# Kernel tuning notes

Measured on AMD Instinct MI355X. Metric: run time of the kernel, lower is better.

## Reference

```python
import jax, jax.numpy as jnp
import numpy as np

EPS = 1e-5  # torch InstanceNorm2d default eps

def conv1x1(x, w, b):
    # x: [B,C,H,W], w: [O,C], b: [O]
    return jnp.einsum('bchw,oc->bohw', x, w) + b[None, :, None, None]

def instance_norm(x):
    # InstanceNorm2d(affine=False): normalize per-sample, per-channel over H,W
    mean = jnp.mean(x, axis=(2, 3), keepdims=True)
    var = jnp.var(x, axis=(2, 3), keepdims=True)
    return (x - mean) * jax.lax.rsqrt(var + EPS)

def proj(x, w, b):
    return jax.nn.relu(instance_norm(conv1x1(x, w, b)))

def setup_inputs() -> dict:
    key = jax.random.key(0)
    ks = jax.random.split(key, 9)
    B, C, Ci, H, W = 16, 256, 128, 64, 64
    s_in = 1.0 / np.sqrt(C)
    s_mid = 1.0 / np.sqrt(Ci)
    return {
        'x': jax.random.normal(ks[0], (B, C, H, W), jnp.float32),
        'g_w': jax.random.normal(ks[1], (Ci, C), jnp.float32) * s_in,
        'g_b': jax.random.normal(ks[2], (Ci,), jnp.float32) * s_in,
        'theta_w': jax.random.normal(ks[3], (Ci, C), jnp.float32) * s_in,
        'theta_b': jax.random.normal(ks[4], (Ci,), jnp.float32) * s_in,
        'phi_w': jax.random.normal(ks[5], (Ci, C), jnp.float32) * s_in,
        'phi_b': jax.random.normal(ks[6], (Ci,), jnp.float32) * s_in,
        'W_w': jax.random.normal(ks[7], (C, Ci), jnp.float32) * s_mid,
        'W_b': jax.random.normal(ks[8], (C,), jnp.float32) * s_mid,
    }

def reference(x, g_w, g_b, theta_w, theta_b, phi_w, phi_b, W_w, W_b):
    B, C, H, W = x.shape
    Ci = g_w.shape[0]
    N = H * W
    g_x = proj(x, g_w, g_b).reshape(B, Ci, N)        # [B,Ci,N]
    theta_x = proj(x, theta_w, theta_b).reshape(B, Ci, N)
    phi_x = proj(x, phi_w, phi_b).reshape(B, Ci, N)
    # channel-attention Gram matrix [B,Ci,Ci], softmax over last dim
    f = jnp.einsum('bin,bjn->bij', theta_x, phi_x)
    attn = jax.nn.softmax(f, axis=2)
    y = jnp.einsum('bij,bjn->bin', attn, g_x)        # [B,Ci,N]
    # replicate torch permute(0,2,1).contiguous().view(B,Ci,H,W)
    y = jnp.transpose(y, (0, 2, 1)).reshape(B, Ci, H, W)
    y = instance_norm(conv1x1(y, W_w, W_b))
    return y + x
```

## Files before the change

kernel.cpp:

```cpp
#include <hip/hip_runtime.h>

#define DEVINL __device__ __forceinline__

typedef __attribute__((ext_vector_type(8))) short bf8v;
typedef __attribute__((ext_vector_type(4))) float f32x4;
typedef __attribute__((ext_vector_type(8))) unsigned short us8;
typedef __attribute__((ext_vector_type(4))) unsigned short us4;

DEVINL unsigned short f2bf(float f) {
  unsigned int u = __builtin_bit_cast(unsigned int, f);
  u += 0x7fffu + ((u >> 16) & 1u);
  return (unsigned short)(u >> 16);
}
DEVINL unsigned short f2bf_trunc(float f) {
  return (unsigned short)(__builtin_bit_cast(unsigned int, f) >> 16);
}
DEVINL float bf2f(unsigned short h) {
  unsigned int u = ((unsigned int)h) << 16;
  return __builtin_bit_cast(float, u);
}

__global__ __launch_bounds__(512, 2)
void proj_gemm(const unsigned short* __restrict__ wall_hi,
               const unsigned short* __restrict__ wall_lo,
               const float* __restrict__ x, float* __restrict__ z)
{
  __shared__ __align__(16) unsigned short As_hi[384 * 72];
  __shared__ __align__(16) unsigned short As_lo[256 * 72];
  __shared__ __align__(16) unsigned short Bs_hi[128 * 72];
  __shared__ __align__(16) unsigned short Bs_lo[128 * 72];

  const int t = threadIdx.x;
  const int lane = t & 63;
  const int wave = t >> 6;
  const int wm = wave >> 1, wn = wave & 1;
  const int lr = lane & 15, lk = lane >> 4;
  const int b = blockIdx.z;
  const int nbase = blockIdx.x * 128;
  const float* xs = x + (long)b * 256 * 4096;

  f32x4 acc[6][4];
#pragma unroll
  for (int i = 0; i < 6; ++i)
#pragma unroll
    for (int j = 0; j < 4; ++j) acc[i][j] = (f32x4)0.0f;

  for (int kt = 0; kt < 4; ++kt) {
    const int k0 = kt * 64;
#pragma unroll
    for (int i = 0; i < 6; ++i) {
      const int q = i * 512 + t;
      const int row = q >> 3, c = q & 7;
      *(us8*)&As_hi[row * 72 + c * 8] = *(const us8*)&wall_hi[(long)row * 256 + k0 + c * 8];
    }
#pragma unroll
    for (int i = 0; i < 4; ++i) {
      const int q = i * 512 + t;
      const int row = q >> 3, c = q & 7;
      *(us8*)&As_lo[row * 72 + c * 8] = *(const us8*)&wall_lo[(long)row * 256 + k0 + c * 8];
    }
    const int nl = t & 127, cg = t >> 7;
    float xv[16];
#pragma unroll
    for (int i = 0; i < 16; ++i)
      xv[i] = xs[(long)(k0 + cg * 16 + i) * 4096 + nbase + nl];
#pragma unroll
    for (int ch = 0; ch < 2; ++ch) {
      us8 h8, l8;
#pragma unroll
      for (int e = 0; e < 8; ++e) {
        const float v = xv[ch * 8 + e];
        const unsigned short hb = f2bf(v);
        h8[e] = hb;
        l8[e] = f2bf_trunc(v - bf2f(hb));
      }
      *(us8*)&Bs_hi[nl * 72 + cg * 16 + ch * 8] = h8;
      *(us8*)&Bs_lo[nl * 72 + cg * 16 + ch * 8] = l8;
    }
    __syncthreads();
#pragma unroll
    for (int ks = 0; ks < 2; ++ks) {
      const int ko = ks * 32 + lk * 8;
      bf8v bh[4], bl[4];
#pragma unroll
      for (int ni = 0; ni < 4; ++ni) {
        const int r = (wn * 64 + ni * 16 + lr) * 72 + ko;
        bh[ni] = *(const bf8v*)&Bs_hi[r];
        bl[ni] = *(const bf8v*)&Bs_lo[r];
      }
#pragma unroll
      for (int mi = 0; mi < 6; ++mi) {
        const int fr = mi * 4 + wm;
        const int r = (fr * 16 + lr) * 72 + ko;
        const bf8v ah = *(const bf8v*)&As_hi[r];
        if (fr < 16) {
          const bf8v al = *(const bf8v*)&As_lo[r];
#pragma unroll
          for (int ni = 0; ni < 4; ++ni) {
            acc[mi][ni] = __builtin_amdgcn_mfma_f32_16x16x32_bf16(bh[ni], ah, acc[mi][ni], 0, 0, 0);
            acc[mi][ni] = __builtin_amdgcn_mfma_f32_16x16x32_bf16(bl[ni], ah, acc[mi][ni], 0, 0, 0);
            acc[mi][ni] = __builtin_amdgcn_mfma_f32_16x16x32_bf16(bh[ni], al, acc[mi][ni], 0, 0, 0);
          }
        } else {
#pragma unroll
          for (int ni = 0; ni < 4; ++ni)
            acc[mi][ni] = __builtin_amdgcn_mfma_f32_16x16x32_bf16(bh[ni], ah, acc[mi][ni], 0, 0, 0);
        }
      }
    }
    __syncthreads();
  }
#pragma unroll
  for (int mi = 0; mi < 6; ++mi)
#pragma unroll
    for (int ni = 0; ni < 4; ++ni) {
      const int gm = (mi * 4 + wm) * 16 + lr;
      const int gn = nbase + wn * 64 + ni * 16 + lk * 4;
      *(f32x4*)&z[((long)b * 384 + gm) * 4096 + gn] = acc[mi][ni];
    }
}

template<int PASSES, bool OUT_BF16>
__global__ __launch_bounds__(256, 2)
void gemm_tn(const unsigned short* __restrict__ Ahi, const unsigned short* __restrict__ Alo,
             const unsigned short* __restrict__ Bhi, const unsigned short* __restrict__ Blo,
             void* __restrict__ Cout,
             int lda, int ldb, int ldc, int ksteps, int z1count,
             long aS1, long aS2, long bS1, long bS2, long cS1, long cS2)
{
  __shared__ __align__(16) unsigned short smem[(PASSES == 3 ? 4 : 2) * 128 * 72];
  unsigned short* As_hi = smem;
  unsigned short* Bs_hi = smem + 128 * 72;
  unsigned short* As_lo = smem + 2 * 128 * 72;
  unsigned short* Bs_lo = smem + 3 * 128 * 72;

  const int t = threadIdx.x;
  const int lane = t & 63;
  const int wave = t >> 6;
  const int wm = wave >> 1, wn = wave & 1;
  const int lr = lane & 15, lk = lane >> 4;

  const int z = blockIdx.z;
  const int zb = z / z1count, z1 = z - zb * z1count;
  const unsigned short* Ah = Ahi + zb * aS2 + z1 * aS1;
  const unsigned short* Bh = Bhi + zb * bS2 + z1 * bS1;
  const unsigned short* Al = (PASSES == 3) ? (Alo + zb * aS2 + z1 * aS1) : nullptr;
  const unsigned short* Bl = (PASSES == 3) ? (Blo + zb * bS2 + z1 * bS1) : nullptr;
  const long cOff = zb * cS2 + z1 * cS1;

  const int mbase = blockIdx.y * 128;
  const int nbase = blockIdx.x * 128;

  f32x4 acc[4][4];
#pragma unroll
  for (int i = 0; i < 4; ++i)
#pragma unroll
    for (int j = 0; j < 4; ++j) acc[i][j] = (f32x4)0.0f;

  for (int kt = 0; kt < ksteps; ++kt) {
    const int k0 = kt * 64;
#pragma unroll
    for (int i = 0; i < 4; ++i) {
      const int q = i * 256 + t;
      const int row = q >> 3, c = q & 7;
      const int lo = row * 72 + c * 8;
      *(us8*)&As_hi[lo] = *(const us8*)&Ah[(long)(mbase + row) * lda + k0 + c * 8];
      *(us8*)&Bs_hi[lo] = *(const us8*)&Bh[(long)(nbase + row) * ldb + k0 + c * 8];
      if (PASSES == 3) {
        *(us8*)&As_lo[lo] = *(const us8*)&Al[(long)(mbase + row) * lda + k0 + c * 8];
        *(us8*)&Bs_lo[lo] = *(const us8*)&Bl[(long)(nbase + row) * ldb + k0 + c * 8];
      }
    }
    __syncthreads();
#pragma unroll
    for (int ks = 0; ks < 2; ++ks) {
      const int ko = ks * 32 + lk * 8;
      bf8v ah[4], bh[4], al[4], bl[4];
#pragma unroll
      for (int mi = 0; mi < 4; ++mi) {
        const int r = (wm * 64 + mi * 16 + lr) * 72 + ko;
        ah[mi] = *(const bf8v*)&As_hi[r];
        if (PASSES == 3) al[mi] = *(const bf8v*)&As_lo[r];
      }
#pragma unroll
      for (int ni = 0; ni < 4; ++ni) {
        const int r = (wn * 64 + ni * 16 + lr) * 72 + ko;
        bh[ni] = *(const bf8v*)&Bs_hi[r];
        if (PASSES == 3) bl[ni] = *(const bf8v*)&Bs_lo[r];
      }
#pragma unroll
      for (int mi = 0; mi < 4; ++mi)
#pragma unroll
        for (int ni = 0; ni < 4; ++ni) {
          acc[mi][ni] = __builtin_amdgcn_mfma_f32_16x16x32_bf16(bh[ni], ah[mi], acc[mi][ni], 0, 0, 0);
          if (PASSES == 3) {
            acc[mi][ni] = __builtin_amdgcn_mfma_f32_16x16x32_bf16(bl[ni], ah[mi], acc[mi][ni], 0, 0, 0);
            acc[mi][ni] = __builtin_amdgcn_mfma_f32_16x16x32_bf16(bh[ni], al[mi], acc[mi][ni], 0, 0, 0);
          }
        }
    }
    __syncthreads();
  }

#pragma unroll
  for (int mi = 0; mi < 4; ++mi)
#pragma unroll
    for (int ni = 0; ni < 4; ++ni) {
      const int gm = mbase + wm * 64 + mi * 16 + lr;
      const int gn = nbase + wn * 64 + ni * 16 + lk * 4;
      const f32x4 v = acc[mi][ni];
      if (OUT_BF16) {
        us4 o;
#pragma unroll
        for (int r = 0; r < 4; ++r) o[r] = f2bf(v[r]);
        *(us4*)&((unsigned short*)Cout)[cOff + (long)gm * ldc + gn] = o;
      } else {
        *(f32x4*)&((float*)Cout)[cOff + (long)gm * ldc + gn] = v;
      }
    }
}

__global__ __launch_bounds__(256)
void prep_weights(const float* __restrict__ g_w, const float* __restrict__ th_w,
                  const float* __restrict__ ph_w, const float* __restrict__ W_w,
                  unsigned short* __restrict__ wall_hi, unsigned short* __restrict__ wall_lo,
                  unsigned short* __restrict__ w2h)
{
  const int i = blockIdx.x * 256 + threadIdx.x;
  float v;
  if (i < 32768) v = th_w[i];
  else if (i < 65536) v = ph_w[i - 32768];
  else v = g_w[i - 65536];
  const unsigned short h = f2bf(v);
  wall_hi[i] = h;
  if (i < 65536) wall_lo[i] = f2bf_trunc(v - bf2f(h));
  if (i < 32768) w2h[i] = f2bf(W_w[i]);
}

__global__ __launch_bounds__(256)
void norm_split(const float* __restrict__ z,
                unsigned short* __restrict__ nhi, unsigned short* __restrict__ nlo)
{
  const int row = blockIdx.x;
  const int b = row >> 8, m = row & 255;
  const float* src = z + ((long)b * 384 + m) * 4096;
  const int t = threadIdx.x;
  f32x4 v[4];
  float s = 0.f, ss = 0.f;
#pragma unroll
  for (int i = 0; i < 4; ++i) {
    v[i] = *(const f32x4*)&src[i * 1024 + t * 4];
#pragma unroll
    for (int e = 0; e < 4; ++e) { s += v[i][e]; ss += v[i][e] * v[i][e]; }
  }
  __shared__ float r0[256], r1[256];
  r0[t] = s; r1[t] = ss;
  __syncthreads();
  for (int o = 128; o > 0; o >>= 1) {
    if (t < o) { r0[t] += r0[t + o]; r1[t] += r1[t + o]; }
    __syncthreads();
  }
  const float mean = r0[0] * (1.f / 4096.f);
  const float var = r1[0] * (1.f / 4096.f) - mean * mean;
  const float rs = rsqrtf(fmaxf(var, 0.f) + 1e-5f);
  const long obase = (long)row * 4096;
#pragma unroll
  for (int i = 0; i < 4; ++i) {
    us4 hi, lo;
#pragma unroll
    for (int e = 0; e < 4; ++e) {
      const float nv = fmaxf((v[i][e] - mean) * rs, 0.f);
      const unsigned short h = f2bf(nv);
      hi[e] = h;
      lo[e] = f2bf_trunc(nv - bf2f(h));
    }
    *(us4*)&nhi[obase + i * 1024 + t * 4] = hi;
    *(us4*)&nlo[obase + i * 1024 + t * 4] = lo;
  }
}

__global__ __launch_bounds__(256)
void stats_g(const float* __restrict__ z, float* __restrict__ statsg)
{
  const int row = blockIdx.x;
  const int b = row >> 7, j = row & 127;
  const float* src = z + ((long)b * 384 + 256 + j) * 4096;
  const int t = threadIdx.x;
  float s = 0.f, ss = 0.f;
#pragma unroll
  for (int i = 0; i < 4; ++i) {
    f32x4 v = *(const f32x4*)&src[i * 1024 + t * 4];
#pragma unroll
    for (int e = 0; e < 4; ++e) { s += v[e]; ss += v[e] * v[e]; }
  }
  __shared__ float r0[256], r1[256];
  r0[t] = s; r1[t] = ss;
  __syncthreads();
  for (int o = 128; o > 0; o >>= 1) {
    if (t < o) { r0[t] += r0[t + o]; r1[t] += r1[t + o]; }
    __syncthreads();
  }
  if (t == 0) {
    const float mean = r0[0] * (1.f / 4096.f);
    const float var = r1[0] * (1.f / 4096.f) - mean * mean;
    statsg[row * 2] = mean;
    statsg[row * 2 + 1] = rsqrtf(fmaxf(var, 0.f) + 1e-5f);
  }
}

__global__ __launch_bounds__(256)
void norm_transpose_g(const float* __restrict__ z, const float* __restrict__ statsg,
                      unsigned short* __restrict__ gT)
{
  __shared__ unsigned short T[64 * 136];
  const int b = blockIdx.y, n0 = blockIdx.x * 64;
  const int t = threadIdx.x;
  const int c = t >> 1, part = t & 1;
  const float mu = statsg[(b * 128 + c) * 2];
  const float rs = statsg[(b * 128 + c) * 2 + 1];
  const float* src = z + ((long)b * 384 + 256 + c) * 4096 + n0 + part * 32;
#pragma unroll
  for (int j = 0; j < 8; ++j) {
    f32x4 v = *(const f32x4*)&src[j * 4];
#pragma unroll
    for (int e = 0; e < 4; ++e) {
      const float nv = fmaxf((v[e] - mu) * rs, 0.f);
      T[(part * 32 + j * 4 + e) * 136 + c] = f2bf(nv);
    }
  }
  __syncthreads();
  const int nl = t >> 2, q = t & 3;
  const long obase = ((long)b * 4096 + n0 + nl) * 128 + q * 32;
#pragma unroll
  for (int k = 0; k < 4; ++k) {
    us8 o;
#pragma unroll
    for (int e = 0; e < 8; ++e) o[e] = T[nl * 136 + q * 32 + k * 8 + e];
    *(us8*)&gT[obase + k * 8] = o;
  }
}

__global__ __launch_bounds__(64)
void softmax_attn(const float* __restrict__ fpart, unsigned short* __restrict__ attn)
{
  const int row = blockIdx.x;
  const int b = row >> 7, i = row & 127;
  const int t = threadIdx.x;
  float v0 = 0.f, v1 = 0.f;
#pragma unroll
  for (int kc = 0; kc < 32; ++kc) {
    const float* p = fpart + ((long)(b * 32 + kc)) * 16384 + i * 128;
    v0 += p[t];
    v1 += p[t + 64];
  }
  float mx = fmaxf(v0, v1);
  for (int o = 32; o > 0; o >>= 1) mx = fmaxf(mx, __shfl_xor(mx, o));
  const float e0 = __expf(v0 - mx), e1 = __expf(v1 - mx);
  float s = e0 + e1;
  for (int o = 32; o > 0; o >>= 1) s += __shfl_xor(s, o);
  const float inv = 1.f / s;
  attn[(long)row * 128 + t] = f2bf(e0 * inv);
  attn[(long)row * 128 + t + 64] = f2bf(e1 * inv);
}

__global__ __launch_bounds__(256)
void finalize(const unsigned short* __restrict__ z2b, const float* __restrict__ x,
              float* __restrict__ out)
{
  const int row = blockIdx.x;
  const long base = (long)row * 4096;
  const int t = threadIdx.x;
  float v[16];
  float s = 0.f, ss = 0.f;
#pragma unroll
  for (int h = 0; h < 2; ++h) {
    us8 u = *(const us8*)&z2b[base + t * 16 + h * 8];
#pragma unroll
    for (int e = 0; e < 8; ++e) {
      const float f = bf2f(u[e]);
      v[h * 8 + e] = f;
      s += f; ss += f * f;
    }
  }
  __shared__ float r0[256], r1[256];
  r0[t] = s; r1[t] = ss;
  __syncthreads();
  for (int o = 128; o > 0; o >>= 1) {
    if (t < o) { r0[t] += r0[t + o]; r1[t] += r1[t + o]; }
    __syncthreads();
  }
  const float mean = r0[0] * (1.f / 4096.f);
  const float var = r1[0] * (1.f / 4096.f) - mean * mean;
  const float rs = rsqrtf(fmaxf(var, 0.f) + 1e-5f);
#pragma unroll
  for (int i = 0; i < 4; ++i) {
    f32x4 xr = *(const f32x4*)&x[base + t * 16 + i * 4];
    f32x4 o;
#pragma unroll
    for (int e = 0; e < 4; ++e) o[e] = (v[i * 4 + e] - mean) * rs + xr[e];
    *(f32x4*)&out[base + t * 16 + i * 4] = o;
  }
}

extern "C" void kernel_launch(void* const* d_in, const int* in_sizes, int n_in,
                              void* d_out, int out_size, void* d_ws, size_t ws_size,
                              hipStream_t stream)
{
  const float* x    = (const float*)d_in[0];
  const float* g_w  = (const float*)d_in[1];
  const float* th_w = (const float*)d_in[3];
  const float* ph_w = (const float*)d_in[5];
  const float* W_w  = (const float*)d_in[7];

  char* ws = (char*)d_ws;
  const size_t MB = 1024ull * 1024ull;
  if (ws_size < 186 * MB) return;

  unsigned short* znorm_hi = (unsigned short*)(ws);
  unsigned short* znorm_lo = (unsigned short*)(ws + 32 * MB);
  float*          z_all    = (float*)(ws + 64 * MB);
  float*          fpart    = (float*)(ws + 64 * MB);
  unsigned short* attn     = (unsigned short*)(ws + 96 * MB);
  unsigned short* y4T      = (unsigned short*)(ws + 98 * MB);
  unsigned short* z2b      = (unsigned short*)(ws + 114 * MB);
  unsigned short* gT       = (unsigned short*)(ws + 160 * MB);
  unsigned short* wall_hi  = (unsigned short*)(ws + 176 * MB);
  unsigned short* wall_lo  = (unsigned short*)(ws + 176 * MB + 256 * 1024);
  unsigned short* w2h      = (unsigned short*)(ws + 176 * MB + 512 * 1024);
  float*          statsg   = (float*)(ws + 176 * MB + 640 * 1024);

  prep_weights<<<dim3(384), 256, 0, stream>>>(g_w, th_w, ph_w, W_w, wall_hi, wall_lo, w2h);

  proj_gemm<<<dim3(32, 1, 16), 512, 0, stream>>>(wall_hi, wall_lo, x, z_all);

  norm_split<<<dim3(4096), 256, 0, stream>>>(z_all, znorm_hi, znorm_lo);

  stats_g<<<dim3(2048), 256, 0, stream>>>(z_all, statsg);
  norm_transpose_g<<<dim3(64, 16), 256, 0, stream>>>(z_all, statsg, gT);

  gemm_tn<3, false><<<dim3(1, 1, 512), 256, 0, stream>>>(
      znorm_hi, znorm_lo, znorm_hi + (long)128 * 4096, znorm_lo + (long)128 * 4096, fpart,
      4096, 4096, 128, 2, 32,
      128, (long)256 * 4096, 128, (long)256 * 4096, 16384, 524288);

  softmax_attn<<<dim3(2048), 64, 0, stream>>>(fpart, attn);

  gemm_tn<1, true><<<dim3(1, 1, 512), 256, 0, stream>>>(
      attn, nullptr, gT, nullptr, y4T,
      128, 4096, 128, 2, 32,
      0, 16384, 128, (long)4096 * 128, 16384, (long)4096 * 128);

  gemm_tn<1, true><<<dim3(32, 2, 16), 256, 0, stream>>>(
      w2h, nullptr, y4T, nullptr, z2b,
      128, 128, 4096, 2, 1,
      0, 0, 0, (long)4096 * 128, 0, (long)256 * 4096);

  finalize<<<dim3(4096), 256, 0, stream>>>(z2b, x, (float*)d_out);
}
```

Before: 181.1 us.

## Fuse instance-norm stats into projection GEMM and normalize on load in Gram GEMM

The projection GEMM now uses smaller N tiles (64 wide, K step 32) and writes its output as bf16 hi/lo pairs instead of fp32. It also emits per-tile sum and sum-of-squares partials, and a tiny kernel reduces them into per-channel scale and shift. The separate norm_split and stats_g passes are removed: the Gram GEMM applies normalize+ReLU+split while loading tiles, and the g transpose reads the hi/lo output. This removes full fp32 intermediate round trips, at the cost of one-pass variance with a bf16-pair representation and redundant normalization work inside the GEMM loads.

```diff
diff --git a/kernel.cpp b/kernel.cpp
--- a/kernel.cpp
+++ b/kernel.cpp
@@ -20,15 +20,17 @@
   return __builtin_bit_cast(float, u);
 }
 
-__global__ __launch_bounds__(512, 2)
+__global__ __launch_bounds__(512, 4)
 void proj_gemm(const unsigned short* __restrict__ wall_hi,
                const unsigned short* __restrict__ wall_lo,
-               const float* __restrict__ x, float* __restrict__ z)
-{
-  __shared__ __align__(16) unsigned short As_hi[384 * 72];
-  __shared__ __align__(16) unsigned short As_lo[256 * 72];
-  __shared__ __align__(16) unsigned short Bs_hi[128 * 72];
-  __shared__ __align__(16) unsigned short Bs_lo[128 * 72];
+               const float* __restrict__ x,
+               unsigned short* __restrict__ zr_hi, unsigned short* __restrict__ zr_lo,
+               float* __restrict__ partials)
+{
+  __shared__ __align__(16) unsigned short As_hi[384 * 40];
+  __shared__ __align__(16) unsigned short As_lo[256 * 40];
+  __shared__ __align__(16) unsigned short Bs_hi[64 * 40];
+  __shared__ __align__(16) unsigned short Bs_lo[64 * 40];
 
   const int t = threadIdx.x;
   const int lane = t & 63;
@@ -36,116 +38,253 @@
   const int wm = wave >> 1, wn = wave & 1;
   const int lr = lane & 15, lk = lane >> 4;
   const int b = blockIdx.z;
-  const int nbase = blockIdx.x * 128;
+  const int bx = blockIdx.x;
+  const int nbase = bx * 64;
   const float* xs = x + (long)b * 256 * 4096;
 
-  f32x4 acc[6][4];
+  f32x4 acc[6][2];
 #pragma unroll
   for (int i = 0; i < 6; ++i)
 #pragma unroll
-    for (int j = 0; j < 4; ++j) acc[i][j] = (f32x4)0.0f;
-
-  for (int kt = 0; kt < 4; ++kt) {
-    const int k0 = kt * 64;
-#pragma unroll
-    for (int i = 0; i < 6; ++i) {
+    for (int j = 0; j < 2; ++j) acc[i][j] = (f32x4)0.0f;
+
+  for (int kt = 0; kt < 8; ++kt) {
+    const int k0 = kt * 32;
+#pragma unroll
+    for (int i = 0; i < 3; ++i) {
       const int q = i * 512 + t;
-      const int row = q >> 3, c = q & 7;
-      *(us8*)&As_hi[row * 72 + c * 8] = *(const us8*)&wall_hi[(long)row * 256 + k0 + c * 8];
-    }
-#pragma unroll
-    for (int i = 0; i < 4; ++i) {
+      const int row = q >> 2, c = q & 3;
+      *(us8*)&As_hi[row * 40 + c * 8] = *(const us8*)&wall_hi[(long)row * 256 + k0 + c * 8];
+    }
+#pragma unroll
+    for (int i = 0; i < 2; ++i) {
       const int q = i * 512 + t;
-      const int row = q >> 3, c = q & 7;
-      *(us8*)&As_lo[row * 72 + c * 8] = *(const us8*)&wall_lo[(long)row * 256 + k0 + c * 8];
-    }
-    const int nl = t & 127, cg = t >> 7;
-    float xv[16];
-#pragma unroll
-    for (int i = 0; i < 16; ++i)
-      xv[i] = xs[(long)(k0 + cg * 16 + i) * 4096 + nbase + nl];
-#pragma unroll
-    for (int ch = 0; ch < 2; ++ch) {
-      us8 h8, l8;
-#pragma unroll
-      for (int e = 0; e < 8; ++e) {
-        const float v = xv[ch * 8 + e];
-        const unsigned short hb = f2bf(v);
-        h8[e] = hb;
-        l8[e] = f2bf_trunc(v - bf2f(hb));
-      }
-      *(us8*)&Bs_hi[nl * 72 + cg * 16 + ch * 8] = h8;
-      *(us8*)&Bs_lo[nl * 72 + cg * 16 + ch * 8] = l8;
-    }
-    __syncthreads();
-#pragma unroll
-    for (int ks = 0; ks < 2; ++ks) {
-      const int ko = ks * 32 + lk * 8;
-      bf8v bh[4], bl[4];
-#pragma unroll
-      for (int ni = 0; ni < 4; ++ni) {
-        const int r = (wn * 64 + ni * 16 + lr) * 72 + ko;
-        bh[ni] = *(const bf8v*)&Bs_hi[r];
-        bl[ni] = *(const bf8v*)&Bs_lo[r];
-      }
-#pragma unroll
-      for (int mi = 0; mi < 6; ++mi) {
-        const int fr = mi * 4 + wm;
-        const int r = (fr * 16 + lr) * 72 + ko;
-        const bf8v ah = *(const bf8v*)&As_hi[r];
-        if (fr < 16) {
-          const bf8v al = *(const bf8v*)&As_lo[r];
-#pragma unroll
-          for (int ni = 0; ni < 4; ++ni) {
-            acc[mi][ni] = __builtin_amdgcn_mfma_f32_16x16x32_bf16(bh[ni], ah, acc[mi][ni], 0, 0, 0);
-            acc[mi][ni] = __builtin_amdgcn_mfma_f32_16x16x32_bf16(bl[ni], ah, acc[mi][ni], 0, 0, 0);
-            acc[mi][ni] = __builtin_amdgcn_mfma_f32_16x16x32_bf16(bh[ni], al, acc[mi][ni], 0, 0, 0);
-          }
-        } else {
-#pragma unroll
-          for (int ni = 0; ni < 4; ++ni)
-            acc[mi][ni] = __builtin_amdgcn_mfma_f32_16x16x32_bf16(bh[ni], ah, acc[mi][ni], 0, 0, 0);
+      const int row = q >> 2, c = q & 3;
+      *(us8*)&As_lo[row * 40 + c * 8] = *(const us8*)&wall_lo[(long)row * 256 + k0 + c * 8];
+    }
+    const int nl = t & 63, cg = t >> 6;
+    float xv[4];
+#pragma unroll
+    for (int i = 0; i < 4; ++i)
+      xv[i] = xs[(long)(k0 + cg * 4 + i) * 4096 + nbase + nl];
+    us4 h4, l4;
+#pragma unroll
+    for (int e = 0; e < 4; ++e) {
+      const float v = xv[e];
+      const unsigned short hb = f2bf(v);
+      h4[e] = hb;
+      l4[e] = f2bf_trunc(v - bf2f(hb));
+    }
+    *(us4*)&Bs_hi[nl * 40 + cg * 4] = h4;
+    *(us4*)&Bs_lo[nl * 40 + cg * 4] = l4;
+    __syncthreads();
+
+    const int ko = lk * 8;
+    bf8v bh[2], bl[2];
+#pragma unroll
+    for (int ni = 0; ni < 2; ++ni) {
+      const int r = (wn * 32 + ni * 16 + lr) * 40 + ko;
+      bh[ni] = *(const bf8v*)&Bs_hi[r];
+      bl[ni] = *(const bf8v*)&Bs_lo[r];
+    }
+#pragma unroll
+    for (int mi = 0; mi < 6; ++mi) {
+      const int fr = mi * 4 + wm;
+      const int r = (fr * 16 + lr) * 40 + ko;
+      const bf8v ah = *(const bf8v*)&As_hi[r];
+      if (fr < 16) {
+        const bf8v al = *(const bf8v*)&As_lo[r];
+#pragma unroll
+        for (int ni = 0; ni < 2; ++ni) {
+          acc[mi][ni] = __builtin_amdgcn_mfma_f32_16x16x32_bf16(bh[ni], ah, acc[mi][ni], 0, 0, 0);
+          acc[mi][ni] = __builtin_amdgcn_mfma_f32_16x16x32_bf16(bl[ni], ah, acc[mi][ni], 0, 0, 0);
+          acc[mi][ni] = __builtin_amdgcn_mfma_f32_16x16x32_bf16(bh[ni], al, acc[mi][ni], 0, 0, 0);
         }
-      }
-    }
-    __syncthreads();
-  }
+      } else {
+#pragma unroll
+        for (int ni = 0; ni < 2; ++ni)
+          acc[mi][ni] = __builtin_amdgcn_mfma_f32_16x16x32_bf16(bh[ni], ah, acc[mi][ni], 0, 0, 0);
+      }
+    }
+    __syncthreads();
+  }
+
+  float* sbuf = (float*)As_hi;
+#pragma unroll
+  for (int mi = 0; mi < 6; ++mi) {
+    float s = 0.f, ss = 0.f;
+#pragma unroll
+    for (int ni = 0; ni < 2; ++ni)
+#pragma unroll
+      for (int r = 0; r < 4; ++r) {
+        const float v = acc[mi][ni][r];
+        s += v; ss += v * v;
+      }
+    const int fr = mi * 4 + wm;
+    const int slot = ((fr * 16 + lr) * 8 + (wn * 4 + lk)) * 2;
+    sbuf[slot] = s; sbuf[slot + 1] = ss;
+  }
+  __syncthreads();
+  if (t < 384) {
+    float s = 0.f, ss = 0.f;
+#pragma unroll
+    for (int w = 0; w < 8; ++w) {
+      s += sbuf[(t * 8 + w) * 2];
+      ss += sbuf[(t * 8 + w) * 2 + 1];
+    }
+    const long pidx = ((long)bx * 6144 + b * 384 + t) * 2;
+    partials[pidx] = s; partials[pidx + 1] = ss;
+  }
+
 #pragma unroll
   for (int mi = 0; mi < 6; ++mi)
 #pragma unroll
-    for (int ni = 0; ni < 4; ++ni) {
+    for (int ni = 0; ni < 2; ++ni) {
       const int gm = (mi * 4 + wm) * 16 + lr;
-      const int gn = nbase + wn * 64 + ni * 16 + lk * 4;
-      *(f32x4*)&z[((long)b * 384 + gm) * 4096 + gn] = acc[mi][ni];
-    }
-}
-
-template<int PASSES, bool OUT_BF16>
-__global__ __launch_bounds__(256, 2)
-void gemm_tn(const unsigned short* __restrict__ Ahi, const unsigned short* __restrict__ Alo,
-             const unsigned short* __restrict__ Bhi, const unsigned short* __restrict__ Blo,
-             void* __restrict__ Cout,
-             int lda, int ldb, int ldc, int ksteps, int z1count,
-             long aS1, long aS2, long bS1, long bS2, long cS1, long cS2)
-{
-  __shared__ __align__(16) unsigned short smem[(PASSES == 3 ? 4 : 2) * 128 * 72];
-  unsigned short* As_hi = smem;
-  unsigned short* Bs_hi = smem + 128 * 72;
-  unsigned short* As_lo = smem + 2 * 128 * 72;
-  unsigned short* Bs_lo = smem + 3 * 128 * 72;
+      const int gn = nbase + wn * 32 + ni * 16 + lk * 4;
+      const long o = ((long)b * 384 + gm) * 4096 + gn;
+      us4 hv, lv;
+#pragma unroll
+      for (int r = 0; r < 4; ++r) {
+        const float v = acc[mi][ni][r];
+        const unsigned short h = f2bf(v);
+        hv[r] = h;
+        lv[r] = f2bf_trunc(v - bf2f(h));
+      }
+      *(us4*)&zr_hi[o] = hv;
+      *(us4*)&zr_lo[o] = lv;
+    }
+}
+
+__global__ __launch_bounds__(256)
+void stats_reduce(const float* __restrict__ partials, float* __restrict__ stats)
+{
+  const int row = blockIdx.x * 256 + threadIdx.x;
+  float s = 0.f, ss = 0.f;
+#pragma unroll
+  for (int k = 0; k < 64; ++k) {
+    s += partials[((long)k * 6144 + row) * 2];
+    ss += partials[((long)k * 6144 + row) * 2 + 1];
+  }
+  const float mean = s * (1.f / 4096.f);
+  const float var = ss * (1.f / 4096.f) - mean * mean;
+  const float rs = rsqrtf(fmaxf(var, 0.f) + 1e-5f);
+  stats[row * 2] = rs;
+  stats[row * 2 + 1] = -mean * rs;
+}
+
+__global__ __launch_bounds__(256, 4)
+void fgemm_norm(const unsigned short* __restrict__ zr_hi, const unsigned short* __restrict__ zr_lo,
+                const float* __restrict__ stats, float* __restrict__ fpart)
+{
+  __shared__ __align__(16) unsigned short As_hi[128 * 72];
+  __shared__ __align__(16) unsigned short As_lo[128 * 72];
+  __shared__ __align__(16) unsigned short Bs_hi[128 * 72];
+  __shared__ __align__(16) unsigned short Bs_lo[128 * 72];
 
   const int t = threadIdx.x;
   const int lane = t & 63;
   const int wave = t >> 6;
   const int wm = wave >> 1, wn = wave & 1;
   const int lr = lane & 15, lk = lane >> 4;
+  const int zb = blockIdx.z >> 5, z1 = blockIdx.z & 31;
+  const int koff = z1 * 128;
+
+  f32x4 acc[4][4];
+#pragma unroll
+  for (int i = 0; i < 4; ++i)
+#pragma unroll
+    for (int j = 0; j < 4; ++j) acc[i][j] = (f32x4)0.0f;
+
+  for (int kt = 0; kt < 2; ++kt) {
+    const int k0 = koff + kt * 64;
+#pragma unroll
+    for (int i = 0; i < 4; ++i) {
+      const int q = i * 256 + t;
+      const int row = q >> 3, c = q & 7;
+#pragma unroll
+      for (int op = 0; op < 2; ++op) {
+        const int grow = zb * 384 + op * 128 + row;
+        const long g = (long)grow * 4096 + k0 + c * 8;
+        const us8 h = *(const us8*)&zr_hi[g];
+        const us8 l = *(const us8*)&zr_lo[g];
+        const float rs = stats[grow * 2];
+        const float nmrs = stats[grow * 2 + 1];
+        us8 oh, ol;
+#pragma unroll
+        for (int e = 0; e < 8; ++e) {
+          const float v = bf2f(h[e]) + bf2f(l[e]);
+          const float nv = fmaxf(__builtin_fmaf(v, rs, nmrs), 0.f);
+          const unsigned short hb = f2bf(nv);
+          oh[e] = hb;
+          ol[e] = f2bf_trunc(nv - bf2f(hb));
+        }
+        unsigned short* dh = op ? Bs_hi : As_hi;
+        unsigned short* dl = op ? Bs_lo : As_lo;
+        *(us8*)&dh[row * 72 + c * 8] = oh;
+        *(us8*)&dl[row * 72 + c * 8] = ol;
+      }
+    }
+    __syncthreads();
+#pragma unroll
+    for (int ks = 0; ks < 2; ++ks) {
+      const int ko = ks * 32 + lk * 8;
+      bf8v ah[4], bh[4], al[4], bl[4];
+#pragma unroll
+      for (int mi = 0; mi < 4; ++mi) {
+        const int r = (wm * 64 + mi * 16 + lr) * 72 + ko;
+        ah[mi] = *(const bf8v*)&As_hi[r];
+        al[mi] = *(const bf8v*)&As_lo[r];
+      }
+#pragma unroll
+      for (int ni = 0; ni < 4; ++ni) {
+        const int r = (wn * 64 + ni * 16 + lr) * 72 + ko;
+        bh[ni] = *(const bf8v*)&Bs_hi[r];
+        bl[ni] = *(const bf8v*)&Bs_lo[r];
+      }
+#pragma unroll
+      for (int mi = 0; mi < 4; ++mi)
+#pragma unroll
+        for (int ni = 0; ni < 4; ++ni) {
+          acc[mi][ni] = __builtin_amdgcn_mfma_f32_16x16x32_bf16(bh[ni], ah[mi], acc[mi][ni], 0, 0, 0);
+          acc[mi][ni] = __builtin_amdgcn_mfma_f32_16x16x32_bf16(bl[ni], ah[mi], acc[mi][ni], 0, 0, 0);
+          acc[mi][ni] = __builtin_amdgcn_mfma_f32_16x16x32_bf16(bh[ni], al[mi], acc[mi][ni], 0, 0, 0);
+        }
+    }
+    __syncthreads();
+  }
+
+  const long cOff = ((long)zb * 32 + z1) * 16384;
+#pragma unroll
+  for (int mi = 0; mi < 4; ++mi)
+#pragma unroll
+    for (int ni = 0; ni < 4; ++ni) {
+      const int gm = wm * 64 + mi * 16 + lr;
+      const int gn = wn * 64 + ni * 16 + lk * 4;
+      *(f32x4*)&fpart[cOff + (long)gm * 128 + gn] = acc[mi][ni];
+    }
+}
+
+template<bool OUT_BF16>
+__global__ __launch_bounds__(256, 2)
+void gemm_tn(const unsigned short* __restrict__ Ah0, const unsigned short* __restrict__ Bh0,
+             void* __restrict__ Cout,
+             int lda, int ldb, int ldc, int ksteps, int z1count,
+             long aS1, long aS2, long bS1, long bS2, long cS1, long cS2)
+{
+  __shared__ __align__(16) unsigned short As_hi[128 * 72];
+  __shared__ __align__(16) unsigned short Bs_hi[128 * 72];
+
+  const int t = threadIdx.x;
+  const int lane = t & 63;
+  const int wave = t >> 6;
+  const int wm = wave >> 1, wn = wave & 1;
+  const int lr = lane & 15, lk = lane >> 4;
 
   const int z = blockIdx.z;
   const int zb = z / z1count, z1 = z - zb * z1count;
-  const unsigned short* Ah = Ahi + zb * aS2 + z1 * aS1;
-  const unsigned short* Bh = Bhi + zb * bS2 + z1 * bS1;
-  const unsigned short* Al = (PASSES == 3) ? (Alo + zb * aS2 + z1 * aS1) : nullptr;
-  const unsigned short* Bl = (PASSES == 3) ? (Blo + zb * bS2 + z1 * bS1) : nullptr;
+  const unsigned short* Ah = Ah0 + zb * aS2 + z1 * aS1;
+  const unsigned short* Bh = Bh0 + zb * bS2 + z1 * bS1;
   const long cOff = zb * cS2 + z1 * cS1;
 
   const int mbase = blockIdx.y * 128;
@@ -166,38 +305,23 @@
       const int lo = row * 72 + c * 8;
       *(us8*)&As_hi[lo] = *(const us8*)&Ah[(long)(mbase + row) * lda + k0 + c * 8];
       *(us8*)&Bs_hi[lo] = *(const us8*)&Bh[(long)(nbase + row) * ldb + k0 + c * 8];
-      if (PASSES == 3) {
-        *(us8*)&As_lo[lo] = *(const us8*)&Al[(long)(mbase + row) * lda + k0 + c * 8];
-        *(us8*)&Bs_lo[lo] = *(const us8*)&Bl[(long)(nbase + row) * ldb + k0 + c * 8];
-      }
     }
     __syncthreads();
 #pragma unroll
     for (int ks = 0; ks < 2; ++ks) {
       const int ko = ks * 32 + lk * 8;
-      bf8v ah[4], bh[4], al[4], bl[4];
-#pragma unroll
-      for (int mi = 0; mi < 4; ++mi) {
-        const int r = (wm * 64 + mi * 16 + lr) * 72 + ko;
-        ah[mi] = *(const bf8v*)&As_hi[r];
-        if (PASSES == 3) al[mi] = *(const bf8v*)&As_lo[r];
-      }
-#pragma unroll
-      for (int ni = 0; ni < 4; ++ni) {
-        const int r = (wn * 64 + ni * 16 + lr) * 72 + ko;
-        bh[ni] = *(const bf8v*)&Bs_hi[r];
-        if (PASSES == 3) bl[ni] = *(const bf8v*)&Bs_lo[r];
-      }
+      bf8v ah[4], bh[4];
 #pragma unroll
       for (int mi = 0; mi < 4; ++mi)
-#pragma unroll
-        for (int ni = 0; ni < 4; ++ni) {
+        ah[mi] = *(const bf8v*)&As_hi[(wm * 64 + mi * 16 + lr) * 72 + ko];
+#pragma unroll
+      for (int ni = 0; ni < 4; ++ni)
+        bh[ni] = *(const bf8v*)&Bs_hi[(wn * 64 + ni * 16 + lr) * 72 + ko];
+#pragma unroll
+      for (int mi = 0; mi < 4; ++mi)
+#pragma unroll
+        for (int ni = 0; ni < 4; ++ni)
           acc[mi][ni] = __builtin_amdgcn_mfma_f32_16x16x32_bf16(bh[ni], ah[mi], acc[mi][ni], 0, 0, 0);
-          if (PASSES == 3) {
-            acc[mi][ni] = __builtin_amdgcn_mfma_f32_16x16x32_bf16(bl[ni], ah[mi], acc[mi][ni], 0, 0, 0);
-            acc[mi][ni] = __builtin_amdgcn_mfma_f32_16x16x32_bf16(bh[ni], al[mi], acc[mi][ni], 0, 0, 0);
-          }
-        }
     }
     __syncthreads();
   }
@@ -238,93 +362,27 @@
 }
 
 __global__ __launch_bounds__(256)
-void norm_split(const float* __restrict__ z,
-                unsigned short* __restrict__ nhi, unsigned short* __restrict__ nlo)
-{
-  const int row = blockIdx.x;
-  const int b = row >> 8, m = row & 255;
-  const float* src = z + ((long)b * 384 + m) * 4096;
-  const int t = threadIdx.x;
-  f32x4 v[4];
-  float s = 0.f, ss = 0.f;
-#pragma unroll
-  for (int i = 0; i < 4; ++i) {
-    v[i] = *(const f32x4*)&src[i * 1024 + t * 4];
-#pragma unroll
-    for (int e = 0; e < 4; ++e) { s += v[i][e]; ss += v[i][e] * v[i][e]; }
-  }
-  __shared__ float r0[256], r1[256];
-  r0[t] = s; r1[t] = ss;
-  __syncthreads();
-  for (int o = 128; o > 0; o >>= 1) {
-    if (t < o) { r0[t] += r0[t + o]; r1[t] += r1[t + o]; }
-    __syncthreads();
-  }
-  const float mean = r0[0] * (1.f / 4096.f);
-  const float var = r1[0] * (1.f / 4096.f) - mean * mean;
-  const float rs = rsqrtf(fmaxf(var, 0.f) + 1e-5f);
-  const long obase = (long)row * 4096;
-#pragma unroll
-  for (int i = 0; i < 4; ++i) {
-    us4 hi, lo;
-#pragma unroll
-    for (int e = 0; e < 4; ++e) {
-      const float nv = fmaxf((v[i][e] - mean) * rs, 0.f);
-      const unsigned short h = f2bf(nv);
-      hi[e] = h;
-      lo[e] = f2bf_trunc(nv - bf2f(h));
-    }
-    *(us4*)&nhi[obase + i * 1024 + t * 4] = hi;
-    *(us4*)&nlo[obase + i * 1024 + t * 4] = lo;
-  }
-}
-
-__global__ __launch_bounds__(256)
-void stats_g(const float* __restrict__ z, float* __restrict__ statsg)
-{
-  const int row = blockIdx.x;
-  const int b = row >> 7, j = row & 127;
-  const float* src = z + ((long)b * 384 + 256 + j) * 4096;
-  const int t = threadIdx.x;
-  float s = 0.f, ss = 0.f;
-#pragma unroll
-  for (int i = 0; i < 4; ++i) {
-    f32x4 v = *(const f32x4*)&src[i * 1024 + t * 4];
-#pragma unroll
-    for (int e = 0; e < 4; ++e) { s += v[e]; ss += v[e] * v[e]; }
-  }
-  __shared__ float r0[256], r1[256];
-  r0[t] = s; r1[t] = ss;
-  __syncthreads();
-  for (int o = 128; o > 0; o >>= 1) {
-    if (t < o) { r0[t] += r0[t + o]; r1[t] += r1[t + o]; }
-    __syncthreads();
-  }
-  if (t == 0) {
-    const float mean = r0[0] * (1.f / 4096.f);
-    const float var = r1[0] * (1.f / 4096.f) - mean * mean;
-    statsg[row * 2] = mean;
-    statsg[row * 2 + 1] = rsqrtf(fmaxf(var, 0.f) + 1e-5f);
-  }
-}
-
-__global__ __launch_bounds__(256)
-void norm_transpose_g(const float* __restrict__ z, const float* __restrict__ statsg,
+void norm_transpose_g(const unsigned short* __restrict__ zr_hi,
+                      const unsigned short* __restrict__ zr_lo,
+                      const float* __restrict__ stats,
                       unsigned short* __restrict__ gT)
 {
   __shared__ unsigned short T[64 * 136];
   const int b = blockIdx.y, n0 = blockIdx.x * 64;
   const int t = threadIdx.x;
   const int c = t >> 1, part = t & 1;
-  const float mu = statsg[(b * 128 + c) * 2];
-  const float rs = statsg[(b * 128 + c) * 2 + 1];
-  const float* src = z + ((long)b * 384 + 256 + c) * 4096 + n0 + part * 32;
+  const int grow = b * 384 + 256 + c;
+  const float rs = stats[grow * 2];
+  const float nmrs = stats[grow * 2 + 1];
+  const long off = (long)grow * 4096 + n0 + part * 32;
 #pragma unroll
   for (int j = 0; j < 8; ++j) {
-    f32x4 v = *(const f32x4*)&src[j * 4];
+    const us4 h = *(const us4*)&zr_hi[off + j * 4];
+    const us4 l = *(const us4*)&zr_lo[off + j * 4];
 #pragma unroll
     for (int e = 0; e < 4; ++e) {
-      const float nv = fmaxf((v[e] - mu) * rs, 0.f);
+      const float v = bf2f(h[e]) + bf2f(l[e]);
+      const float nv = fmaxf(__builtin_fmaf(v, rs, nmrs), 0.f);
       T[(part * 32 + j * 4 + e) * 136 + c] = f2bf(nv);
     }
   }
@@ -416,42 +474,38 @@
   const size_t MB = 1024ull * 1024ull;
   if (ws_size < 186 * MB) return;
 
-  unsigned short* znorm_hi = (unsigned short*)(ws);
-  unsigned short* znorm_lo = (unsigned short*)(ws + 32 * MB);
-  float*          z_all    = (float*)(ws + 64 * MB);
-  float*          fpart    = (float*)(ws + 64 * MB);
-  unsigned short* attn     = (unsigned short*)(ws + 96 * MB);
-  unsigned short* y4T      = (unsigned short*)(ws + 98 * MB);
-  unsigned short* z2b      = (unsigned short*)(ws + 114 * MB);
-  unsigned short* gT       = (unsigned short*)(ws + 160 * MB);
-  unsigned short* wall_hi  = (unsigned short*)(ws + 176 * MB);
-  unsigned short* wall_lo  = (unsigned short*)(ws + 176 * MB + 256 * 1024);
-  unsigned short* w2h      = (unsigned short*)(ws + 176 * MB + 512 * 1024);
-  float*          statsg   = (float*)(ws + 176 * MB + 640 * 1024);
+  unsigned short* zr_hi    = (unsigned short*)(ws);
+  unsigned short* zr_lo    = (unsigned short*)(ws + 48 * MB);
+  float*          fpart    = (float*)(ws + 96 * MB);
+  unsigned short* attn     = (unsigned short*)(ws + 128 * MB);
+  unsigned short* gT       = (unsigned short*)(ws + 132 * MB);
+  unsigned short* y4T      = (unsigned short*)(ws + 148 * MB);
+  unsigned short* z2b      = (unsigned short*)(ws);
+  float*          partials = (float*)(ws + 164 * MB);
+  float*          stats    = (float*)(ws + 167 * MB);
+  unsigned short* wall_hi  = (unsigned short*)(ws + 168 * MB);
+  unsigned short* wall_lo  = (unsigned short*)(ws + 168 * MB + 256 * 1024);
+  unsigned short* w2h      = (unsigned short*)(ws + 168 * MB + 512 * 1024);
 
   prep_weights<<<dim3(384), 256, 0, stream>>>(g_w, th_w, ph_w, W_w, wall_hi, wall_lo, w2h);
 
-  proj_gemm<<<dim3(32, 1, 16), 512, 0, stream>>>(wall_hi, wall_lo, x, z_all);
-
-  norm_split<<<dim3(4096), 256, 0, stream>>>(z_all, znorm_hi, znorm_lo);
-
-  stats_g<<<dim3(2048), 256, 0, stream>>>(z_all, statsg);
-  norm_transpose_g<<<dim3(64, 16), 256, 0, stream>>>(z_all, statsg, gT);
-
-  gemm_tn<3, false><<<dim3(1, 1, 512), 256, 0, stream>>>(
-      znorm_hi, znorm_lo, znorm_hi + (long)128 * 4096, znorm_lo + (long)128 * 4096, fpart,
-      4096, 4096, 128, 2, 32,
-      128, (long)256 * 4096, 128, (long)256 * 4096, 16384, 524288);
+  proj_gemm<<<dim3(64, 1, 16), 512, 0, stream>>>(wall_hi, wall_lo, x, zr_hi, zr_lo, partials);
+
+  stats_reduce<<<dim3(24), 256, 0, stream>>>(partials, stats);
+
+  norm_transpose_g<<<dim3(64, 16), 256, 0, stream>>>(zr_hi, zr_lo, stats, gT);
+
+  fgemm_norm<<<dim3(1, 1, 512), 256, 0, stream>>>(zr_hi, zr_lo, stats, fpart);
 
   softmax_attn<<<dim3(2048), 64, 0, stream>>>(fpart, attn);
 
-  gemm_tn<1, true><<<dim3(1, 1, 512), 256, 0, stream>>>(
-      attn, nullptr, gT, nullptr, y4T,
+  gemm_tn<true><<<dim3(1, 1, 512), 256, 0, stream>>>(
+      attn, gT, y4T,
       128, 4096, 128, 2, 32,
       0, 16384, 128, (long)4096 * 128, 16384, (long)4096 * 128);
 
-  gemm_tn<1, true><<<dim3(32, 2, 16), 256, 0, stream>>>(
-      w2h, nullptr, y4T, nullptr, z2b,
+  gemm_tn<true><<<dim3(32, 2, 16), 256, 0, stream>>>(
+      w2h, y4T, z2b,
       128, 128, 4096, 2, 1,
       0, 0, 0, (long)4096 * 128, 0, (long)256 * 4096);
 
```

New measurement: 174.4 us. 1.04x faster.
